# Optimization experiments

Hardware: AMD Instinct MI355X
Metric: run time of the kernel (lower is better)

The kernel has to match this reference:

```python
import jax, jax.numpy as jnp
import numpy as np

HIDDEN = 512
LATENT = 256
NUM_NODE_TYPES = 16


def setup_inputs() -> dict:
    key = jax.random.key(0)
    ks = jax.random.split(key, 9)
    s = lambda fan_in: 1.0 / np.sqrt(fan_in)
    return {
        "z": jax.random.normal(ks[0], (1024, LATENT), dtype=jnp.float32),
        "num_nodes": 128,
        "W_z": jax.random.uniform(ks[1], (LATENT, HIDDEN), jnp.float32, -s(LATENT), s(LATENT)),
        "b_z": jax.random.uniform(ks[2], (HIDDEN,), jnp.float32, -s(LATENT), s(LATENT)),
        "W_node": jax.random.uniform(ks[3], (HIDDEN, NUM_NODE_TYPES), jnp.float32, -s(HIDDEN), s(HIDDEN)),
        "b_node": jax.random.uniform(ks[4], (NUM_NODE_TYPES,), jnp.float32, -s(HIDDEN), s(HIDDEN)),
        "W_e1": jax.random.uniform(ks[5], (2 * HIDDEN, HIDDEN), jnp.float32, -s(2 * HIDDEN), s(2 * HIDDEN)),
        "b_e1": jax.random.uniform(ks[6], (HIDDEN,), jnp.float32, -s(2 * HIDDEN), s(2 * HIDDEN)),
        "W_e2": jax.random.uniform(ks[7], (HIDDEN, 1), jnp.float32, -s(HIDDEN), s(HIDDEN)),
        "b_e2": jax.random.uniform(ks[8], (1,), jnp.float32, -s(HIDDEN), s(HIDDEN)),
    }


def reference(z, num_nodes, W_z, b_z, W_node, b_node, W_e1, b_e1, W_e2, b_e2):
    # h: [B, H]
    h = jax.nn.relu(z @ W_z + b_z)
    B = z.shape[0]
    # h_expanded: [B, N, H] (same h replicated per node, as in the original)
    h_expanded = jnp.broadcast_to(h[:, None, :], (B, num_nodes, h.shape[-1]))
    node_logits = h_expanded @ W_node + b_node  # [B, N, T]
    # Every (i, j) pair in the original loop uses cat(h, h) -> identical scalar per batch.
    h_pair = jnp.concatenate([h, h], axis=-1)  # [B, 2H]
    p = jax.nn.sigmoid(jax.nn.relu(h_pair @ W_e1 + b_e1) @ W_e2 + b_e2)  # [B, 1]
    # Scatter onto strict lower triangle (j < i), zeros elsewhere.
    tril = jnp.tril(jnp.ones((num_nodes, num_nodes), dtype=z.dtype), k=-1)  # [N, N]
    edge_probs = p[:, :, None] * tril[None, :, :]  # [B, N, N]
    return node_logits, edge_probs
```

## Files before the change

### kernel.cpp

```cpp
#include <hip/hip_runtime.h>
#include <hip/hip_bf16.h>
#include <math.h>

#define BB 1024
#define LL 256
#define HH 512
#define TT 16
#define NN 128

#define NODE_F4 (BB * NN * TT / 4)
#define EDGE_F4 (BB * NN * NN / 4)

typedef short bf16x8 __attribute__((ext_vector_type(8)));
typedef float f32x4  __attribute__((ext_vector_type(4)));

static __device__ __forceinline__ short bfbits(float f) {
    __hip_bfloat16 h = __float2bfloat16(f);
    return *reinterpret_cast<short*>(&h);
}

static __device__ __forceinline__ int h_addr(int row, int col) {
    return (row << 10) + ((((col >> 3) ^ (row & 7)) << 4)) + ((col & 7) << 1);
}

__device__ __forceinline__ void transpose_tile(const float* __restrict__ in,
                                               __hip_bfloat16* __restrict__ out,
                                               int k0, int n0, int Kdim, bool fold,
                                               __hip_bfloat16 (*tile)[34]) {
    const int tx = threadIdx.x & 31;
    const int ty = threadIdx.x >> 5;
    #pragma unroll
    for (int r = ty; r < 32; r += 8) {
        float v = in[(k0 + r) * HH + n0 + tx];
        if (fold) v += in[(k0 + r + HH) * HH + n0 + tx];
        tile[r][tx] = __float2bfloat16(v);
    }
    __syncthreads();
    #pragma unroll
    for (int r = ty; r < 32; r += 8) {
        out[(n0 + r) * Kdim + k0 + tx] = tile[tx][r];
    }
}

__global__ __launch_bounds__(256) void k_prep(const float* __restrict__ Wz,
                                              const float* __restrict__ We1,
                                              const float* __restrict__ Wn,
                                              __hip_bfloat16* __restrict__ WzT,
                                              __hip_bfloat16* __restrict__ WsumT,
                                              __hip_bfloat16* __restrict__ WnT) {
    __shared__ __hip_bfloat16 tile[32][34];
    const int bid = blockIdx.x;
    const int tid = threadIdx.x;
    if (bid < 128) {
        transpose_tile(Wz, WzT, (bid >> 4) * 32, (bid & 15) * 32, LL, false, tile);
    } else if (bid < 384) {
        const int t = bid - 128;
        transpose_tile(We1, WsumT, (t >> 4) * 32, (t & 15) * 32, HH, true, tile);
    } else {
        const int u = (bid - 384) * 256 + tid;
        const int tt = u >> 9, k = u & 511;
        WnT[u] = __float2bfloat16(Wn[k * TT + tt]);
    }
}

__global__ __launch_bounds__(512) void k_fused(const float* __restrict__ z,
                                               const __hip_bfloat16* __restrict__ WzT,
                                               const __hip_bfloat16* __restrict__ WsumT,
                                               const __hip_bfloat16* __restrict__ WnT,
                                               const float* __restrict__ bz,
                                               const float* __restrict__ be1,
                                               const float* __restrict__ We2,
                                               const float* __restrict__ bn,
                                               const float* __restrict__ be2,
                                               float* __restrict__ node16,
                                               float* __restrict__ p) {
    __shared__ char  hbuf[16384];
    __shared__ f32x4 nod_lds[8][64];
    __shared__ float pw_lds[8][16];

    const int w    = threadIdx.x >> 6;
    const int lane = threadIdx.x & 63;
    const int l16  = lane & 15, quad = lane >> 4;
    const int r0   = blockIdx.x << 4;

    bf16x8 afr[8];
    {
        const float4* zf = (const float4*)(z + (r0 + l16) * LL);
        #pragma unroll
        for (int kt = 0; kt < 8; ++kt) {
            float4 v0 = zf[quad * 2 + kt * 8];
            float4 v1 = zf[quad * 2 + kt * 8 + 1];
            bf16x8 a;
            a[0] = bfbits(v0.x); a[1] = bfbits(v0.y); a[2] = bfbits(v0.z); a[3] = bfbits(v0.w);
            a[4] = bfbits(v1.x); a[5] = bfbits(v1.y); a[6] = bfbits(v1.z); a[7] = bfbits(v1.w);
            afr[kt] = a;
        }
    }
    #pragma unroll
    for (int i = 0; i < 4; ++i) {
        const int nt = (w << 2) + i;
        const short* Bp = (const short*)WzT + (nt * 16 + l16) * LL + quad * 8;
        f32x4 acc = {0.f, 0.f, 0.f, 0.f};
        #pragma unroll
        for (int kt = 0; kt < 8; ++kt) {
            bf16x8 b = *(const bf16x8*)(Bp + kt * 32);
            acc = __builtin_amdgcn_mfma_f32_16x16x32_bf16(afr[kt], b, acc, 0, 0, 0);
        }
        const int col = nt * 16 + l16;
        const float bb = bz[col];
        #pragma unroll
        for (int r = 0; r < 4; ++r) {
            float hv = fmaxf(acc[r] + bb, 0.f);
            *(short*)(hbuf + h_addr(quad * 4 + r, col)) = bfbits(hv);
        }
    }
    __syncthreads();

    {
        f32x4 acc = {0.f, 0.f, 0.f, 0.f};
        const short* Bp = (const short*)WnT + l16 * HH + quad * 8;
        #pragma unroll
        for (int kk = 0; kk < 2; ++kk) {
            const int kt = w * 2 + kk;
            bf16x8 a = *(const bf16x8*)(hbuf + h_addr(l16, quad * 8 + kt * 32));
            bf16x8 b = *(const bf16x8*)(Bp + kt * 32);
            acc = __builtin_amdgcn_mfma_f32_16x16x32_bf16(a, b, acc, 0, 0, 0);
        }
        nod_lds[w][lane] = acc;
    }

    {
        f32x4 acc[4];
        #pragma unroll
        for (int i = 0; i < 4; ++i) acc[i] = (f32x4){0.f, 0.f, 0.f, 0.f};
        #pragma unroll
        for (int kt = 0; kt < 16; ++kt) {
            bf16x8 a = *(const bf16x8*)(hbuf + h_addr(l16, quad * 8 + kt * 32));
            #pragma unroll
            for (int i = 0; i < 4; ++i) {
                const int nt = (w << 2) + i;
                bf16x8 b = *(const bf16x8*)((const short*)WsumT +
                            (nt * 16 + l16) * HH + quad * 8 + kt * 32);
                acc[i] = __builtin_amdgcn_mfma_f32_16x16x32_bf16(a, b, acc[i], 0, 0, 0);
            }
        }
        float psum[4] = {0.f, 0.f, 0.f, 0.f};
        #pragma unroll
        for (int i = 0; i < 4; ++i) {
            const int col = ((w << 2) + i) * 16 + l16;
            const float bb = be1[col], w2 = We2[col];
            float sr[4];
            #pragma unroll
            for (int r = 0; r < 4; ++r) sr[r] = fmaxf(acc[i][r] + bb, 0.f) * w2;
            #pragma unroll
            for (int off = 1; off < 16; off <<= 1) {
                #pragma unroll
                for (int r = 0; r < 4; ++r) sr[r] += __shfl_xor(sr[r], off);
            }
            #pragma unroll
            for (int r = 0; r < 4; ++r) psum[r] += sr[r];
        }
        if (l16 == 0) {
            #pragma unroll
            for (int r = 0; r < 4; ++r) pw_lds[w][quad * 4 + r] = psum[r];
        }
    }
    __syncthreads();

    if (w == 0) {
        f32x4 s = nod_lds[0][lane];
        #pragma unroll
        for (int ww = 1; ww < 8; ++ww) {
            f32x4 t = nod_lds[ww][lane];
            s[0] += t[0]; s[1] += t[1]; s[2] += t[2]; s[3] += t[3];
        }
        const float bb = bn[l16];
        #pragma unroll
        for (int r = 0; r < 4; ++r)
            node16[(r0 + quad * 4 + r) * TT + l16] = s[r] + bb;
    } else if (w == 1 && lane < 16) {
        float t = 0.f;
        #pragma unroll
        for (int ww = 0; ww < 8; ++ww) t += pw_lds[ww][lane];
        t += be2[0];
        p[r0 + lane] = 1.f / (1.f + expf(-t));
    }
}

__global__ __launch_bounds__(256) void k_write(const float* __restrict__ node16,
                                               const float* __restrict__ p,
                                               float4* __restrict__ out) {
    const int q = blockIdx.x * 256 + threadIdx.x;
    if (q < NODE_F4) {
        const int b  = q >> 9;
        const int t4 = q & 3;
        out[q] = ((const float4*)(node16 + b * TT))[t4];
    } else {
        const int e  = q - NODE_F4;
        const int b  = e >> 12;
        const int i  = (e >> 5) & 127;
        const int j0 = (e & 31) * 4;
        const float pv = p[b];
        float4 v;
        v.x = (j0 + 0 < i) ? pv : 0.f;
        v.y = (j0 + 1 < i) ? pv : 0.f;
        v.z = (j0 + 2 < i) ? pv : 0.f;
        v.w = (j0 + 3 < i) ? pv : 0.f;
        out[q] = v;
    }
}

extern "C" void kernel_launch(void* const* d_in, const int* in_sizes, int n_in,
                              void* d_out, int out_size, void* d_ws, size_t ws_size,
                              hipStream_t stream) {
    const float* z    = (const float*)d_in[0];
    const float* Wz   = (const float*)d_in[2];
    const float* bz   = (const float*)d_in[3];
    const float* Wn   = (const float*)d_in[4];
    const float* bn   = (const float*)d_in[5];
    const float* We1  = (const float*)d_in[6];
    const float* be1  = (const float*)d_in[7];
    const float* We2  = (const float*)d_in[8];
    const float* be2  = (const float*)d_in[9];
    float* out = (float*)d_out;

    char* base = (char*)d_ws;
    __hip_bfloat16* WzT    = (__hip_bfloat16*)(base);
    __hip_bfloat16* WsumT  = (__hip_bfloat16*)(base +  256 * 1024);
    __hip_bfloat16* WnT    = (__hip_bfloat16*)(base +  768 * 1024);
    float*          node16 = (float*)(base + 784 * 1024);
    float*          p      = (float*)(base + 848 * 1024);

    k_prep<<<416, 256, 0, stream>>>(Wz, We1, Wn, WzT, WsumT, WnT);

    k_fused<<<BB / 16, 512, 0, stream>>>(z, WzT, WsumT, WnT,
                                         bz, be1, We2, bn, be2, node16, p);

    k_write<<<(NODE_F4 + EDGE_F4) / 256, 256, 0, stream>>>(node16, p, (float4*)out);

    (void)in_sizes; (void)n_in; (void)out_size; (void)ws_size;
}
```

Baseline: 134.5 us.

## Fuse prep, MLP and output write into one cooperative kernel with grid syncs

Replaces the three launches (weight transpose, fused MLP, output broadcast) with one cooperative kernel of 256 blocks that uses grid-wide syncs between phases. Each group of four blocks shares a 16-row batch tile, recomputes the first layer redundantly, splits the edge-MLP columns four ways and combines partial sums with atomicAdd. The output write phase then streams the node logits and triangular edge probabilities per batch row. The aim is to remove launch gaps and raise parallelism in the MLP phase. The cost is two grid barriers, four-fold redundant first-layer compute, and an output write limited to 256 blocks, which may reduce write bandwidth for the dominant 64MB store.

Measured after the change: 188.1 us. 39.9% more time.

```diff
diff --git a/kernel.cpp b/kernel.cpp
--- a/kernel.cpp
+++ b/kernel.cpp
@@ -1,6 +1,9 @@
 #include <hip/hip_runtime.h>
 #include <hip/hip_bf16.h>
+#include <hip/hip_cooperative_groups.h>
 #include <math.h>
+
+namespace cg = cooperative_groups;
 
 #define BB 1024
 #define LL 256
@@ -23,68 +26,73 @@
     return (row << 10) + ((((col >> 3) ^ (row & 7)) << 4)) + ((col & 7) << 1);
 }
 
-__device__ __forceinline__ void transpose_tile(const float* __restrict__ in,
-                                               __hip_bfloat16* __restrict__ out,
-                                               int k0, int n0, int Kdim, bool fold,
-                                               __hip_bfloat16 (*tile)[34]) {
-    const int tx = threadIdx.x & 31;
-    const int ty = threadIdx.x >> 5;
-    #pragma unroll
-    for (int r = ty; r < 32; r += 8) {
-        float v = in[(k0 + r) * HH + n0 + tx];
-        if (fold) v += in[(k0 + r + HH) * HH + n0 + tx];
-        tile[r][tx] = __float2bfloat16(v);
-    }
-    __syncthreads();
-    #pragma unroll
-    for (int r = ty; r < 32; r += 8) {
-        out[(n0 + r) * Kdim + k0 + tx] = tile[tx][r];
-    }
-}
-
-__global__ __launch_bounds__(256) void k_prep(const float* __restrict__ Wz,
-                                              const float* __restrict__ We1,
-                                              const float* __restrict__ Wn,
-                                              __hip_bfloat16* __restrict__ WzT,
-                                              __hip_bfloat16* __restrict__ WsumT,
-                                              __hip_bfloat16* __restrict__ WnT) {
+__global__ __launch_bounds__(512) void k_all(const float* __restrict__ z,
+                                             const float* __restrict__ Wz,
+                                             const float* __restrict__ bz,
+                                             const float* __restrict__ Wn,
+                                             const float* __restrict__ bn,
+                                             const float* __restrict__ We1,
+                                             const float* __restrict__ be1,
+                                             const float* __restrict__ We2,
+                                             const float* __restrict__ be2,
+                                             __hip_bfloat16* __restrict__ WzT,
+                                             __hip_bfloat16* __restrict__ WsumT,
+                                             __hip_bfloat16* __restrict__ WnT,
+                                             float* __restrict__ node16,
+                                             float* __restrict__ p_acc,
+                                             float* __restrict__ out) {
     __shared__ __hip_bfloat16 tile[32][34];
-    const int bid = blockIdx.x;
-    const int tid = threadIdx.x;
-    if (bid < 128) {
-        transpose_tile(Wz, WzT, (bid >> 4) * 32, (bid & 15) * 32, LL, false, tile);
-    } else if (bid < 384) {
-        const int t = bid - 128;
-        transpose_tile(We1, WsumT, (t >> 4) * 32, (t & 15) * 32, HH, true, tile);
-    } else {
-        const int u = (bid - 384) * 256 + tid;
-        const int tt = u >> 9, k = u & 511;
-        WnT[u] = __float2bfloat16(Wn[k * TT + tt]);
-    }
-}
-
-__global__ __launch_bounds__(512) void k_fused(const float* __restrict__ z,
-                                               const __hip_bfloat16* __restrict__ WzT,
-                                               const __hip_bfloat16* __restrict__ WsumT,
-                                               const __hip_bfloat16* __restrict__ WnT,
-                                               const float* __restrict__ bz,
-                                               const float* __restrict__ be1,
-                                               const float* __restrict__ We2,
-                                               const float* __restrict__ bn,
-                                               const float* __restrict__ be2,
-                                               float* __restrict__ node16,
-                                               float* __restrict__ p) {
     __shared__ char  hbuf[16384];
     __shared__ f32x4 nod_lds[8][64];
     __shared__ float pw_lds[8][16];
 
-    const int w    = threadIdx.x >> 6;
-    const int lane = threadIdx.x & 63;
+    const int bid = blockIdx.x;
+    const int tid = threadIdx.x;
+    cg::grid_group gg = cg::this_grid();
+
+    {
+        const int tx = tid & 31;
+        const int ty = tid >> 5;
+        for (int t = bid; t < 384; t += 256) {
+            const float* in; __hip_bfloat16* o; int k0, n0, Kdim; bool fold;
+            if (t < 128) {
+                in = Wz;  o = WzT;  k0 = (t >> 4) * 32; n0 = (t & 15) * 32;
+                Kdim = LL; fold = false;
+            } else {
+                const int t2 = t - 128;
+                in = We1; o = WsumT; k0 = (t2 >> 4) * 32; n0 = (t2 & 15) * 32;
+                Kdim = HH; fold = true;
+            }
+            #pragma unroll
+            for (int r = ty; r < 32; r += 16) {
+                float v = in[(k0 + r) * HH + n0 + tx];
+                if (fold) v += in[(k0 + r + HH) * HH + n0 + tx];
+                tile[r][tx] = __float2bfloat16(v);
+            }
+            __syncthreads();
+            #pragma unroll
+            for (int r = ty; r < 32; r += 16)
+                o[(n0 + r) * Kdim + k0 + tx] = tile[tx][r];
+            __syncthreads();
+        }
+        if (bid >= 248) {
+            const int u = (bid - 248) * 1024 + tid;
+            WnT[u]       = __float2bfloat16(Wn[(u & 511) * TT + (u >> 9)]);
+            WnT[u + 512] = __float2bfloat16(Wn[((u + 512) & 511) * TT + ((u + 512) >> 9)]);
+        }
+        if (bid == 247 && tid < 256)
+            ((float4*)p_acc)[tid] = make_float4(0.f, 0.f, 0.f, 0.f);
+    }
+    gg.sync();
+
+    const int w    = tid >> 6;
+    const int lane = tid & 63;
     const int l16  = lane & 15, quad = lane >> 4;
-    const int r0   = blockIdx.x << 4;
-
-    bf16x8 afr[8];
-    {
+    const int g = bid >> 2, q = bid & 3;
+    const int r0 = g << 4;
+
+    {
+        bf16x8 afr[8];
         const float4* zf = (const float4*)(z + (r0 + l16) * LL);
         #pragma unroll
         for (int kt = 0; kt < 8; ++kt) {
@@ -95,28 +103,28 @@
             a[4] = bfbits(v1.x); a[5] = bfbits(v1.y); a[6] = bfbits(v1.z); a[7] = bfbits(v1.w);
             afr[kt] = a;
         }
-    }
-    #pragma unroll
-    for (int i = 0; i < 4; ++i) {
-        const int nt = (w << 2) + i;
-        const short* Bp = (const short*)WzT + (nt * 16 + l16) * LL + quad * 8;
-        f32x4 acc = {0.f, 0.f, 0.f, 0.f};
-        #pragma unroll
-        for (int kt = 0; kt < 8; ++kt) {
-            bf16x8 b = *(const bf16x8*)(Bp + kt * 32);
-            acc = __builtin_amdgcn_mfma_f32_16x16x32_bf16(afr[kt], b, acc, 0, 0, 0);
-        }
-        const int col = nt * 16 + l16;
-        const float bb = bz[col];
-        #pragma unroll
-        for (int r = 0; r < 4; ++r) {
-            float hv = fmaxf(acc[r] + bb, 0.f);
-            *(short*)(hbuf + h_addr(quad * 4 + r, col)) = bfbits(hv);
+        #pragma unroll
+        for (int i = 0; i < 4; ++i) {
+            const int nt = (w << 2) + i;
+            const short* Bp = (const short*)WzT + (nt * 16 + l16) * LL + quad * 8;
+            f32x4 acc = {0.f, 0.f, 0.f, 0.f};
+            #pragma unroll
+            for (int kt = 0; kt < 8; ++kt) {
+                bf16x8 b = *(const bf16x8*)(Bp + kt * 32);
+                acc = __builtin_amdgcn_mfma_f32_16x16x32_bf16(afr[kt], b, acc, 0, 0, 0);
+            }
+            const int col = nt * 16 + l16;
+            const float bb = bz[col];
+            #pragma unroll
+            for (int r = 0; r < 4; ++r) {
+                float hv = fmaxf(acc[r] + bb, 0.f);
+                *(short*)(hbuf + h_addr(quad * 4 + r, col)) = bfbits(hv);
+            }
         }
     }
     __syncthreads();
 
-    {
+    if (q == 3) {
         f32x4 acc = {0.f, 0.f, 0.f, 0.f};
         const short* Bp = (const short*)WnT + l16 * HH + quad * 8;
         #pragma unroll
@@ -130,44 +138,33 @@
     }
 
     {
-        f32x4 acc[4];
-        #pragma unroll
-        for (int i = 0; i < 4; ++i) acc[i] = (f32x4){0.f, 0.f, 0.f, 0.f};
+        const int nt = q * 8 + w;
+        const short* Bp = (const short*)WsumT + (nt * 16 + l16) * HH + quad * 8;
+        f32x4 acc = {0.f, 0.f, 0.f, 0.f};
         #pragma unroll
         for (int kt = 0; kt < 16; ++kt) {
             bf16x8 a = *(const bf16x8*)(hbuf + h_addr(l16, quad * 8 + kt * 32));
-            #pragma unroll
-            for (int i = 0; i < 4; ++i) {
-                const int nt = (w << 2) + i;
-                bf16x8 b = *(const bf16x8*)((const short*)WsumT +
-                            (nt * 16 + l16) * HH + quad * 8 + kt * 32);
-                acc[i] = __builtin_amdgcn_mfma_f32_16x16x32_bf16(a, b, acc[i], 0, 0, 0);
-            }
-        }
-        float psum[4] = {0.f, 0.f, 0.f, 0.f};
-        #pragma unroll
-        for (int i = 0; i < 4; ++i) {
-            const int col = ((w << 2) + i) * 16 + l16;
-            const float bb = be1[col], w2 = We2[col];
-            float sr[4];
-            #pragma unroll
-            for (int r = 0; r < 4; ++r) sr[r] = fmaxf(acc[i][r] + bb, 0.f) * w2;
-            #pragma unroll
-            for (int off = 1; off < 16; off <<= 1) {
-                #pragma unroll
-                for (int r = 0; r < 4; ++r) sr[r] += __shfl_xor(sr[r], off);
-            }
-            #pragma unroll
-            for (int r = 0; r < 4; ++r) psum[r] += sr[r];
+            bf16x8 b = *(const bf16x8*)(Bp + kt * 32);
+            acc = __builtin_amdgcn_mfma_f32_16x16x32_bf16(a, b, acc, 0, 0, 0);
+        }
+        const int col = nt * 16 + l16;
+        const float bb = be1[col], w2 = We2[col];
+        float sr[4];
+        #pragma unroll
+        for (int r = 0; r < 4; ++r) sr[r] = fmaxf(acc[r] + bb, 0.f) * w2;
+        #pragma unroll
+        for (int off = 1; off < 16; off <<= 1) {
+            #pragma unroll
+            for (int r = 0; r < 4; ++r) sr[r] += __shfl_xor(sr[r], off);
         }
         if (l16 == 0) {
             #pragma unroll
-            for (int r = 0; r < 4; ++r) pw_lds[w][quad * 4 + r] = psum[r];
+            for (int r = 0; r < 4; ++r) pw_lds[w][quad * 4 + r] = sr[r];
         }
     }
     __syncthreads();
 
-    if (w == 0) {
+    if (q == 3 && w == 0) {
         f32x4 s = nod_lds[0][lane];
         #pragma unroll
         for (int ww = 1; ww < 8; ++ww) {
@@ -178,35 +175,38 @@
         #pragma unroll
         for (int r = 0; r < 4; ++r)
             node16[(r0 + quad * 4 + r) * TT + l16] = s[r] + bb;
-    } else if (w == 1 && lane < 16) {
+    }
+    if (w == 1 && lane < 16) {
         float t = 0.f;
         #pragma unroll
         for (int ww = 0; ww < 8; ++ww) t += pw_lds[ww][lane];
-        t += be2[0];
-        p[r0 + lane] = 1.f / (1.f + expf(-t));
-    }
-}
-
-__global__ __launch_bounds__(256) void k_write(const float* __restrict__ node16,
-                                               const float* __restrict__ p,
-                                               float4* __restrict__ out) {
-    const int q = blockIdx.x * 256 + threadIdx.x;
-    if (q < NODE_F4) {
-        const int b  = q >> 9;
-        const int t4 = q & 3;
-        out[q] = ((const float4*)(node16 + b * TT))[t4];
-    } else {
-        const int e  = q - NODE_F4;
-        const int b  = e >> 12;
-        const int i  = (e >> 5) & 127;
-        const int j0 = (e & 31) * 4;
-        const float pv = p[b];
-        float4 v;
-        v.x = (j0 + 0 < i) ? pv : 0.f;
-        v.y = (j0 + 1 < i) ? pv : 0.f;
-        v.z = (j0 + 2 < i) ? pv : 0.f;
-        v.w = (j0 + 3 < i) ? pv : 0.f;
-        out[q] = v;
+        atomicAdd(p_acc + r0 + lane, t);
+    }
+    gg.sync();
+
+    {
+        float4* onode = (float4*)out;
+        float4* oedge = (float4*)out + NODE_F4;
+        const float b2 = be2[0];
+        #pragma unroll
+        for (int i = 0; i < 4; ++i) {
+            const int b = r0 + (q << 2) + i;
+            const float pv = 1.f / (1.f + expf(-(p_acc[b] + b2)));
+            float4 nv = ((const float4*)(node16 + b * TT))[tid & 3];
+            onode[b * 512 + tid] = nv;
+            #pragma unroll
+            for (int it = 0; it < 8; ++it) {
+                const int e  = it * 512 + tid;
+                const int ii = e >> 5;
+                const int j0 = (e & 31) << 2;
+                float4 v;
+                v.x = (j0 + 0 < ii) ? pv : 0.f;
+                v.y = (j0 + 1 < ii) ? pv : 0.f;
+                v.z = (j0 + 2 < ii) ? pv : 0.f;
+                v.w = (j0 + 3 < ii) ? pv : 0.f;
+                oedge[b * 4096 + e] = v;
+            }
+        }
     }
 }
 
@@ -229,14 +229,14 @@
     __hip_bfloat16* WsumT  = (__hip_bfloat16*)(base +  256 * 1024);
     __hip_bfloat16* WnT    = (__hip_bfloat16*)(base +  768 * 1024);
     float*          node16 = (float*)(base + 784 * 1024);
-    float*          p      = (float*)(base + 848 * 1024);
-
-    k_prep<<<416, 256, 0, stream>>>(Wz, We1, Wn, WzT, WsumT, WnT);
-
-    k_fused<<<BB / 16, 512, 0, stream>>>(z, WzT, WsumT, WnT,
-                                         bz, be1, We2, bn, be2, node16, p);
-
-    k_write<<<(NODE_F4 + EDGE_F4) / 256, 256, 0, stream>>>(node16, p, (float4*)out);
+    float*          p_acc  = (float*)(base + 848 * 1024);
+
+    void* args[] = { (void*)&z, (void*)&Wz, (void*)&bz, (void*)&Wn, (void*)&bn,
+                     (void*)&We1, (void*)&be1, (void*)&We2, (void*)&be2,
+                     (void*)&WzT, (void*)&WsumT, (void*)&WnT,
+                     (void*)&node16, (void*)&p_acc, (void*)&out };
+    hipLaunchCooperativeKernel((const void*)k_all, dim3(256), dim3(512),
+                               args, 0, stream);
 
     (void)in_sizes; (void)n_in; (void)out_size; (void)ws_size;
 }
```

## Split edge MLP across 4 blocks per row group, fuse node writes, add edge kernel

Applied to the files above, without the earlier changes.

The fused kernel now launches four blocks per 16-row group, and each block computes a quarter of the We1 output columns. The partial edge logits are combined with atomicAdd into a zeroed accumulator, which gives more parallelism than the previous 64 blocks. Node logits are broadcast and written straight from the fused kernel, so the node16 intermediate buffer and its round trip go away. A separate edge kernel applies the sigmoid and writes the triangular output with nontemporal stores, with 8 iterations per thread. The trade-off is redundant h and node computation in each of the four blocks, plus float atomics that make the summation order nondeterministic.

Result: faster. 127.0 us (-5.6%).

```diff
diff --git a/kernel.cpp b/kernel.cpp
--- a/kernel.cpp
+++ b/kernel.cpp
@@ -47,7 +47,8 @@
                                               const float* __restrict__ Wn,
                                               __hip_bfloat16* __restrict__ WzT,
                                               __hip_bfloat16* __restrict__ WsumT,
-                                              __hip_bfloat16* __restrict__ WnT) {
+                                              __hip_bfloat16* __restrict__ WnT,
+                                              float* __restrict__ p_acc) {
     __shared__ __hip_bfloat16 tile[32][34];
     const int bid = blockIdx.x;
     const int tid = threadIdx.x;
@@ -56,10 +57,11 @@
     } else if (bid < 384) {
         const int t = bid - 128;
         transpose_tile(We1, WsumT, (t >> 4) * 32, (t & 15) * 32, HH, true, tile);
-    } else {
+    } else if (bid < 416) {
         const int u = (bid - 384) * 256 + tid;
-        const int tt = u >> 9, k = u & 511;
-        WnT[u] = __float2bfloat16(Wn[k * TT + tt]);
+        WnT[u] = __float2bfloat16(Wn[(u & 511) * TT + (u >> 9)]);
+    } else if (tid < 256) {
+        ((float4*)p_acc)[tid] = make_float4(0.f, 0.f, 0.f, 0.f);
     }
 }
 
@@ -71,20 +73,22 @@
                                                const float* __restrict__ be1,
                                                const float* __restrict__ We2,
                                                const float* __restrict__ bn,
-                                               const float* __restrict__ be2,
-                                               float* __restrict__ node16,
-                                               float* __restrict__ p) {
+                                               float* __restrict__ p_acc,
+                                               float4* __restrict__ out) {
     __shared__ char  hbuf[16384];
     __shared__ f32x4 nod_lds[8][64];
     __shared__ float pw_lds[8][16];
-
-    const int w    = threadIdx.x >> 6;
-    const int lane = threadIdx.x & 63;
+    __shared__ float nodef[16][16];
+
+    const int tid  = threadIdx.x;
+    const int w    = tid >> 6;
+    const int lane = tid & 63;
     const int l16  = lane & 15, quad = lane >> 4;
-    const int r0   = blockIdx.x << 4;
-
-    bf16x8 afr[8];
-    {
+    const int g = blockIdx.x >> 2, q = blockIdx.x & 3;
+    const int r0 = g << 4;
+
+    {
+        bf16x8 afr[8];
         const float4* zf = (const float4*)(z + (r0 + l16) * LL);
         #pragma unroll
         for (int kt = 0; kt < 8; ++kt) {
@@ -95,23 +99,23 @@
             a[4] = bfbits(v1.x); a[5] = bfbits(v1.y); a[6] = bfbits(v1.z); a[7] = bfbits(v1.w);
             afr[kt] = a;
         }
-    }
-    #pragma unroll
-    for (int i = 0; i < 4; ++i) {
-        const int nt = (w << 2) + i;
-        const short* Bp = (const short*)WzT + (nt * 16 + l16) * LL + quad * 8;
-        f32x4 acc = {0.f, 0.f, 0.f, 0.f};
-        #pragma unroll
-        for (int kt = 0; kt < 8; ++kt) {
-            bf16x8 b = *(const bf16x8*)(Bp + kt * 32);
-            acc = __builtin_amdgcn_mfma_f32_16x16x32_bf16(afr[kt], b, acc, 0, 0, 0);
-        }
-        const int col = nt * 16 + l16;
-        const float bb = bz[col];
-        #pragma unroll
-        for (int r = 0; r < 4; ++r) {
-            float hv = fmaxf(acc[r] + bb, 0.f);
-            *(short*)(hbuf + h_addr(quad * 4 + r, col)) = bfbits(hv);
+        #pragma unroll
+        for (int i = 0; i < 4; ++i) {
+            const int nt = (w << 2) + i;
+            const short* Bp = (const short*)WzT + (nt * 16 + l16) * LL + quad * 8;
+            f32x4 acc = {0.f, 0.f, 0.f, 0.f};
+            #pragma unroll
+            for (int kt = 0; kt < 8; ++kt) {
+                bf16x8 b = *(const bf16x8*)(Bp + kt * 32);
+                acc = __builtin_amdgcn_mfma_f32_16x16x32_bf16(afr[kt], b, acc, 0, 0, 0);
+            }
+            const int col = nt * 16 + l16;
+            const float bb = bz[col];
+            #pragma unroll
+            for (int r = 0; r < 4; ++r) {
+                float hv = fmaxf(acc[r] + bb, 0.f);
+                *(short*)(hbuf + h_addr(quad * 4 + r, col)) = bfbits(hv);
+            }
         }
     }
     __syncthreads();
@@ -130,39 +134,28 @@
     }
 
     {
-        f32x4 acc[4];
-        #pragma unroll
-        for (int i = 0; i < 4; ++i) acc[i] = (f32x4){0.f, 0.f, 0.f, 0.f};
+        const int nt = q * 8 + w;
+        const short* Bp = (const short*)WsumT + (nt * 16 + l16) * HH + quad * 8;
+        f32x4 acc = {0.f, 0.f, 0.f, 0.f};
         #pragma unroll
         for (int kt = 0; kt < 16; ++kt) {
             bf16x8 a = *(const bf16x8*)(hbuf + h_addr(l16, quad * 8 + kt * 32));
-            #pragma unroll
-            for (int i = 0; i < 4; ++i) {
-                const int nt = (w << 2) + i;
-                bf16x8 b = *(const bf16x8*)((const short*)WsumT +
-                            (nt * 16 + l16) * HH + quad * 8 + kt * 32);
-                acc[i] = __builtin_amdgcn_mfma_f32_16x16x32_bf16(a, b, acc[i], 0, 0, 0);
-            }
-        }
-        float psum[4] = {0.f, 0.f, 0.f, 0.f};
-        #pragma unroll
-        for (int i = 0; i < 4; ++i) {
-            const int col = ((w << 2) + i) * 16 + l16;
-            const float bb = be1[col], w2 = We2[col];
-            float sr[4];
-            #pragma unroll
-            for (int r = 0; r < 4; ++r) sr[r] = fmaxf(acc[i][r] + bb, 0.f) * w2;
-            #pragma unroll
-            for (int off = 1; off < 16; off <<= 1) {
-                #pragma unroll
-                for (int r = 0; r < 4; ++r) sr[r] += __shfl_xor(sr[r], off);
-            }
-            #pragma unroll
-            for (int r = 0; r < 4; ++r) psum[r] += sr[r];
+            bf16x8 b = *(const bf16x8*)(Bp + kt * 32);
+            acc = __builtin_amdgcn_mfma_f32_16x16x32_bf16(a, b, acc, 0, 0, 0);
+        }
+        const int col = nt * 16 + l16;
+        const float bb = be1[col], w2 = We2[col];
+        float sr[4];
+        #pragma unroll
+        for (int r = 0; r < 4; ++r) sr[r] = fmaxf(acc[r] + bb, 0.f) * w2;
+        #pragma unroll
+        for (int off = 1; off < 16; off <<= 1) {
+            #pragma unroll
+            for (int r = 0; r < 4; ++r) sr[r] += __shfl_xor(sr[r], off);
         }
         if (l16 == 0) {
             #pragma unroll
-            for (int r = 0; r < 4; ++r) pw_lds[w][quad * 4 + r] = psum[r];
+            for (int r = 0; r < 4; ++r) pw_lds[w][quad * 4 + r] = sr[r];
         }
     }
     __syncthreads();
@@ -177,36 +170,48 @@
         const float bb = bn[l16];
         #pragma unroll
         for (int r = 0; r < 4; ++r)
-            node16[(r0 + quad * 4 + r) * TT + l16] = s[r] + bb;
-    } else if (w == 1 && lane < 16) {
+            nodef[quad * 4 + r][l16] = s[r] + bb;
+    }
+    if (w == 1 && lane < 16) {
         float t = 0.f;
         #pragma unroll
         for (int ww = 0; ww < 8; ++ww) t += pw_lds[ww][lane];
-        t += be2[0];
-        p[r0 + lane] = 1.f / (1.f + expf(-t));
-    }
-}
-
-__global__ __launch_bounds__(256) void k_write(const float* __restrict__ node16,
-                                               const float* __restrict__ p,
-                                               float4* __restrict__ out) {
-    const int q = blockIdx.x * 256 + threadIdx.x;
-    if (q < NODE_F4) {
-        const int b  = q >> 9;
-        const int t4 = q & 3;
-        out[q] = ((const float4*)(node16 + b * TT))[t4];
-    } else {
-        const int e  = q - NODE_F4;
+        atomicAdd(p_acc + r0 + lane, t);
+    }
+    __syncthreads();
+
+    {
+        const float4* nf4 = (const float4*)nodef;
+        #pragma unroll
+        for (int i = 0; i < 4; ++i) {
+            const int idx = i * 512 + tid;
+            const int bl  = idx >> 7;
+            const int rem = idx & 127;
+            const int nl  = rem >> 2;
+            const int t4  = rem & 3;
+            out[(r0 + bl) * 512 + (q * 32 + nl) * 4 + t4] = nf4[bl * 4 + t4];
+        }
+    }
+}
+
+__global__ __launch_bounds__(256) void k_edge(const float* __restrict__ p_acc,
+                                              const float* __restrict__ be2,
+                                              f32x4* __restrict__ oedge) {
+    const int gid = blockIdx.x * 256 + threadIdx.x;
+    const float b2 = be2[0];
+    #pragma unroll
+    for (int it = 0; it < 8; ++it) {
+        const int e  = it * (2048 * 256) + gid;
         const int b  = e >> 12;
         const int i  = (e >> 5) & 127;
-        const int j0 = (e & 31) * 4;
-        const float pv = p[b];
-        float4 v;
-        v.x = (j0 + 0 < i) ? pv : 0.f;
-        v.y = (j0 + 1 < i) ? pv : 0.f;
-        v.z = (j0 + 2 < i) ? pv : 0.f;
-        v.w = (j0 + 3 < i) ? pv : 0.f;
-        out[q] = v;
+        const int j0 = (e & 31) << 2;
+        const float pv = 1.f / (1.f + expf(-(p_acc[b] + b2)));
+        f32x4 v;
+        v[0] = (j0 + 0 < i) ? pv : 0.f;
+        v[1] = (j0 + 1 < i) ? pv : 0.f;
+        v[2] = (j0 + 2 < i) ? pv : 0.f;
+        v[3] = (j0 + 3 < i) ? pv : 0.f;
+        __builtin_nontemporal_store(v, oedge + e);
     }
 }
 
@@ -228,15 +233,14 @@
     __hip_bfloat16* WzT    = (__hip_bfloat16*)(base);
     __hip_bfloat16* WsumT  = (__hip_bfloat16*)(base +  256 * 1024);
     __hip_bfloat16* WnT    = (__hip_bfloat16*)(base +  768 * 1024);
-    float*          node16 = (float*)(base + 784 * 1024);
-    float*          p      = (float*)(base + 848 * 1024);
-
-    k_prep<<<416, 256, 0, stream>>>(Wz, We1, Wn, WzT, WsumT, WnT);
-
-    k_fused<<<BB / 16, 512, 0, stream>>>(z, WzT, WsumT, WnT,
-                                         bz, be1, We2, bn, be2, node16, p);
-
-    k_write<<<(NODE_F4 + EDGE_F4) / 256, 256, 0, stream>>>(node16, p, (float4*)out);
+    float*          p_acc  = (float*)(base + 784 * 1024);
+
+    k_prep<<<417, 256, 0, stream>>>(Wz, We1, Wn, WzT, WsumT, WnT, p_acc);
+
+    k_fused<<<256, 512, 0, stream>>>(z, WzT, WsumT, WnT,
+                                     bz, be1, We2, bn, p_acc, (float4*)out);
+
+    k_edge<<<2048, 256, 0, stream>>>(p_acc, be2, (f32x4*)((float4*)out + NODE_F4));
 
     (void)in_sizes; (void)n_in; (void)out_size; (void)ws_size;
 }
```
